# Performance work log

Hardware: AMD Instinct MI355X
Metric: run time of the kernel (lower is better)

Reference implementation:

```python
import jax, jax.numpy as jnp
import numpy as np

E, D, H, K = 8, 2048, 1024, 2  # num_experts, input_size, hidden_size, top_k
B, L = 2, 1024


def setup_inputs() -> dict:
    key = jax.random.key(0)
    k1, k2, k3, k4 = jax.random.split(key, 4)
    x = jax.random.normal(k1, (B, L, D), dtype=jnp.float32)
    w_gate = jax.random.normal(k2, (E, D), dtype=jnp.float32) * 0.02   # router Linear weight [E, D]
    w_in = jax.random.normal(k3, (E, 2 * H, D), dtype=jnp.float32) * 0.02  # ParallelExperts [E, out=2H, in=D]
    w_out = jax.random.normal(k4, (E, D, H), dtype=jnp.float32) * 0.02     # ParallelExperts [E, out=D, in=H]
    bias = jnp.zeros((D,), dtype=jnp.float32)
    return {"x": x, "w_gate": w_gate, "w_in": w_in, "w_out": w_out, "bias": bias}


def _moe_forward(x, w_gate, w_in, w_out, bias):
    bsz, length, d = x.shape
    xt = x.reshape(-1, d)  # [T, D]
    # top-k router: logits -> top-k -> softmax over selected logits
    logits = xt @ w_gate.T  # [T, E]
    topk_vals, topk_idx = jax.lax.top_k(logits, K)  # [T, K]
    topk_gates = jax.nn.softmax(topk_vals, axis=-1)  # [T, K]
    T = xt.shape[0]
    # dense [T, E] gate matrix; zero for non-selected experts, so the dense
    # per-expert compute below is mathematically identical to gathered dispatch
    gates = jnp.zeros((T, E), dtype=xt.dtype).at[jnp.arange(T)[:, None], topk_idx].add(topk_gates)
    # expert GLU FFN, vectorized over experts
    h = jnp.einsum('td,efd->tef', xt, w_in)  # [T, E, 2H]
    h1, h2 = jnp.split(h, 2, axis=-1)
    a = jax.nn.silu(h1) * h2                 # [T, E, H]
    eo = jnp.einsum('teh,edh->ted', a, w_out)  # [T, E, D]
    y = jnp.einsum('ted,te->td', eo, gates) + bias
    return y.reshape(bsz, length, d)


def reference(x, w_gate, w_in, w_out, bias):
    y = _moe_forward(x, w_gate, w_in, w_out, bias)
    loss = jnp.float32(0.0)  # router aux loss is 0 in eval mode (JetMoE top_k_gating)
    return (y, loss)
```

## Files before the change

kernel.cpp:

```cpp
#include <hip/hip_runtime.h>

#define E_    8
#define D_    2048
#define H_    1024
#define T_    2048
#define BK    64
#define NN    32

using u16   = unsigned short;
using s16x8 = __attribute__((ext_vector_type(8))) short;
using f32x4 = __attribute__((ext_vector_type(4))) float;

__device__ __forceinline__ u16 f2bf(float f) {
  union { float f; unsigned u; } v; v.f = f;
  unsigned r = v.u + 0x7fffu + ((v.u >> 16) & 1u);
  return (u16)(r >> 16);
}
__device__ __forceinline__ s16x8 cvt8(f32x4 a, f32x4 b) {
  s16x8 o;
  o[0]=(short)f2bf(a.x); o[1]=(short)f2bf(a.y); o[2]=(short)f2bf(a.z); o[3]=(short)f2bf(a.w);
  o[4]=(short)f2bf(b.x); o[5]=(short)f2bf(b.y); o[6]=(short)f2bf(b.z); o[7]=(short)f2bf(b.w);
  return o;
}
__device__ __forceinline__ int slot(int r, int c) { return r * 64 + ((c ^ (r & 7)) << 3); }

__device__ __forceinline__ void gload16(const void* g, void* l) {
  __builtin_amdgcn_global_load_lds((const __attribute__((address_space(1))) void*)g,
                                   (__attribute__((address_space(3))) void*)l, 16, 0, 0);
}

#define FIND_EXPERT(ml, cnt, e, mt, Ne)                        \
  { int b_ = 0;                                                \
    _Pragma("unroll")                                          \
    for (int i_ = 0; i_ < E_; ++i_) {                          \
      int ti_ = (cnt[i_] + 255) >> 8;                          \
      if ((ml) >= b_ && (ml) < b_ + ti_) {                     \
        e = i_; mt = (ml) - b_; Ne = cnt[i_]; }                \
      b_ += ti_; } }


__global__ __launch_bounds__(256) void init_kernel(
    const float* __restrict__ bias, float* __restrict__ out, int* __restrict__ counts)
{
  int idx = blockIdx.x * 256 + threadIdx.x;
  if (blockIdx.x == 0 && threadIdx.x < E_) counts[threadIdx.x] = 0;
  if (idx == 0) out[(size_t)T_ * D_] = 0.0f;
  int dq = idx & (D_ / 4 - 1);
  f32x4 b = *(const f32x4*)(bias + dq * 4);
  *(f32x4*)(out + (size_t)idx * 4) = b;
}

__global__ __launch_bounds__(256) void router_kernel(
    const float* __restrict__ x, const float* __restrict__ wg,
    u16* __restrict__ xb, int* __restrict__ lists, float* __restrict__ gates,
    int* __restrict__ counts)
{
  int t = blockIdx.x;
  int tid = threadIdx.x;
  const float* xr = x + (size_t)t * D_;
  float acc[E_];
#pragma unroll
  for (int e = 0; e < E_; ++e) acc[e] = 0.f;
#pragma unroll
  for (int i = 0; i < D_ / 256; ++i) {
    int d = tid + 256 * i;
    float xv = xr[d];
    xb[(size_t)t * D_ + d] = f2bf(xv);
#pragma unroll
    for (int e = 0; e < E_; ++e) acc[e] += xv * wg[e * D_ + d];
  }
#pragma unroll
  for (int off = 32; off >= 1; off >>= 1)
#pragma unroll
    for (int e = 0; e < E_; ++e) acc[e] += __shfl_down(acc[e], off);

  __shared__ float red[4][E_];
  int w = tid >> 6, lane = tid & 63;
  if (lane == 0)
#pragma unroll
    for (int e = 0; e < E_; ++e) red[w][e] = acc[e];
  __syncthreads();
  if (tid == 0) {
    float v0 = -1e30f, v1 = -1e30f; int e0 = 0, e1 = 0;
#pragma unroll
    for (int e = 0; e < E_; ++e) {
      float v = red[0][e] + red[1][e] + red[2][e] + red[3][e];
      if (v > v0)      { v1 = v0; e1 = e0; v0 = v; e0 = e; }
      else if (v > v1) { v1 = v;  e1 = e; }
    }
    float g1 = expf(v1 - v0);
    float inv = 1.f / (1.f + g1);
    float g0 = inv; g1 *= inv;
    int s0 = atomicAdd(&counts[e0], 1);
    lists[e0 * T_ + s0] = t * 2 + 0;
    gates[t * 2 + 0] = g0;
    int s1 = atomicAdd(&counts[e1], 1);
    lists[e1 * T_ + s1] = t * 2 + 1;
    gates[t * 2 + 1] = g1;
  }
}

__global__ __launch_bounds__(512, 4) void gemm1_kernel(
    const u16* __restrict__ xb, const float* __restrict__ w_in,
    const int* __restrict__ lists, const int* __restrict__ counts,
    u16* __restrict__ a_buf)
{
  __shared__ __align__(16) u16 As[2][256 * 64];
  __shared__ __align__(16) u16 Bs[2][64 * 64];

  int cnt[E_];
#pragma unroll
  for (int i = 0; i < E_; ++i) cnt[i] = counts[i];
  int mt_total = 0;
#pragma unroll
  for (int i = 0; i < E_; ++i) mt_total += (cnt[i] + 255) >> 8;
  int total = mt_total * NN;
  int chunk = (total + 7) >> 3;

  int tid = threadIdx.x, w = tid >> 6, lane = tid & 63;
  int swzc = ((lane & 7) ^ (lane >> 3)) * 8;
  int brow = tid >> 3, bch = tid & 7;
  int wr = (w >> 1) * 64, wcB = (w & 1) * 32, lrow = lane & 15, g = lane >> 4;
  int lcol = lane & 15, lr4 = (lane >> 4) * 4;

  int xcd = blockIdx.x & 7, bslot = blockIdx.x >> 3;

  for (int sl = bslot; sl < chunk; sl += 64) {
    int t = xcd * chunk + sl;
    if (t >= total) break;
    int ml = t >> 5, n = t & (NN - 1);
    int e = 0, mt = 0, Ne = 0;
    FIND_EXPERT(ml, cnt, e, mt, Ne);

    const u16* ap[4];
#pragma unroll
    for (int i = 0; i < 4; ++i) {
      int gr = mt * 256 + 32 * w + 8 * i + (lane >> 3);
      if (gr >= Ne) gr = Ne - 1;
      ap[i] = xb + (size_t)(lists[e * T_ + gr] >> 1) * D_ + swzc;
    }
    int o = n * 32 + ((brow >> 4) & 1) * H_ + (brow >> 5) * 16 + (brow & 15);
    const float* bp = w_in + (size_t)e * (2 * H_) * D_ + (size_t)o * D_ + bch * 8;

    f32x4 acc[4][2];
#pragma unroll
    for (int m = 0; m < 4; ++m) { acc[m][0] = (f32x4){0,0,0,0}; acc[m][1] = (f32x4){0,0,0,0}; }

    f32x4 bl0 = *(const f32x4*)(bp), bl1 = *(const f32x4*)(bp + 4);
#pragma unroll
    for (int i = 0; i < 4; ++i) gload16(ap[i], &As[0][(32 * w + 8 * i) * 64]);
    *(s16x8*)(&Bs[0][slot(brow, bch)]) = cvt8(bl0, bl1);
    __syncthreads();

    const int NT = D_ / BK;
    for (int kt = 0; kt < NT; ++kt) {
      int cur = kt & 1;
      if (kt + 1 < NT) {
        int k = (kt + 1) * BK;
        bl0 = *(const f32x4*)(bp + k); bl1 = *(const f32x4*)(bp + k + 4);
#pragma unroll
        for (int i = 0; i < 4; ++i) gload16(ap[i] + k, &As[cur ^ 1][(32 * w + 8 * i) * 64]);
      }
#pragma unroll
      for (int ks = 0; ks < 2; ++ks) {
        int ch = ks * 4 + g;
        s16x8 af[4], bf[2];
#pragma unroll
        for (int m = 0; m < 4; ++m) af[m] = *(const s16x8*)(&As[cur][slot(wr + m * 16 + lrow, ch)]);
#pragma unroll
        for (int nn = 0; nn < 2; ++nn) bf[nn] = *(const s16x8*)(&Bs[cur][slot(wcB + nn * 16 + lrow, ch)]);
#pragma unroll
        for (int m = 0; m < 4; ++m)
#pragma unroll
          for (int nn = 0; nn < 2; ++nn)
            acc[m][nn] = __builtin_amdgcn_mfma_f32_16x16x32_bf16(af[m], bf[nn], acc[m][nn], 0, 0, 0);
      }
      if (kt + 1 < NT)
        *(s16x8*)(&Bs[cur ^ 1][slot(brow, bch)]) = cvt8(bl0, bl1);
      __syncthreads();
    }
#pragma unroll
    for (int m = 0; m < 4; ++m)
#pragma unroll
      for (int q = 0; q < 4; ++q) {
        int row = mt * 256 + wr + m * 16 + lr4 + q;
        if (row < Ne) {
          float h1 = acc[m][0][q], h2 = acc[m][1][q];
          float a = (h1 / (1.f + __expf(-h1))) * h2;
          a_buf[((size_t)e * T_ + row) * H_ + n * 32 + (w & 1) * 16 + lcol] = f2bf(a);
        }
      }
  }
}

__global__ __launch_bounds__(512, 4) void gemm2_kernel(
    const u16* __restrict__ a_buf, const float* __restrict__ w_out,
    const int* __restrict__ lists, const int* __restrict__ counts,
    const float* __restrict__ gates, float* __restrict__ out)
{
  __shared__ __align__(16) u16 As[2][256 * 64];
  __shared__ __align__(16) u16 Bs[2][64 * 64];

  int cnt[E_];
#pragma unroll
  for (int i = 0; i < E_; ++i) cnt[i] = counts[i];
  int mt_total = 0;
#pragma unroll
  for (int i = 0; i < E_; ++i) mt_total += (cnt[i] + 255) >> 8;
  int total = mt_total * NN;
  int chunk = (total + 7) >> 3;

  int tid = threadIdx.x, w = tid >> 6, lane = tid & 63;
  int swzc = ((lane & 7) ^ (lane >> 3)) * 8;
  int brow = tid >> 3, bch = tid & 7;
  int wr = (w >> 1) * 64, wcB = (w & 1) * 32, lrow = lane & 15, g = lane >> 4;
  int lcol = lane & 15, lr4 = (lane >> 4) * 4;

  int xcd = blockIdx.x & 7, bslot = blockIdx.x >> 3;

  for (int sl = bslot; sl < chunk; sl += 64) {
    int t = xcd * chunk + sl;
    if (t >= total) break;
    int ml = t >> 5, n = t & (NN - 1);
    int e = 0, mt = 0, Ne = 0;
    FIND_EXPERT(ml, cnt, e, mt, Ne);

    const u16* ap[4];
#pragma unroll
    for (int i = 0; i < 4; ++i) {
      int gr = mt * 256 + 32 * w + 8 * i + (lane >> 3);
      if (gr >= Ne) gr = Ne - 1;
      ap[i] = a_buf + ((size_t)e * T_ + gr) * H_ + swzc;
    }
    const float* bp = w_out + (size_t)e * D_ * H_ + (size_t)(n * 64 + brow) * H_ + bch * 8;

    f32x4 acc[4][2];
#pragma unroll
    for (int m = 0; m < 4; ++m) { acc[m][0] = (f32x4){0,0,0,0}; acc[m][1] = (f32x4){0,0,0,0}; }

    f32x4 bl0 = *(const f32x4*)(bp), bl1 = *(const f32x4*)(bp + 4);
#pragma unroll
    for (int i = 0; i < 4; ++i) gload16(ap[i], &As[0][(32 * w + 8 * i) * 64]);
    *(s16x8*)(&Bs[0][slot(brow, bch)]) = cvt8(bl0, bl1);
    __syncthreads();

    const int NT = H_ / BK;
    for (int kt = 0; kt < NT; ++kt) {
      int cur = kt & 1;
      if (kt + 1 < NT) {
        int k = (kt + 1) * BK;
        bl0 = *(const f32x4*)(bp + k); bl1 = *(const f32x4*)(bp + k + 4);
#pragma unroll
        for (int i = 0; i < 4; ++i) gload16(ap[i] + k, &As[cur ^ 1][(32 * w + 8 * i) * 64]);
      }
#pragma unroll
      for (int ks = 0; ks < 2; ++ks) {
        int ch = ks * 4 + g;
        s16x8 af[4], bf[2];
#pragma unroll
        for (int m = 0; m < 4; ++m) af[m] = *(const s16x8*)(&As[cur][slot(wr + m * 16 + lrow, ch)]);
#pragma unroll
        for (int nn = 0; nn < 2; ++nn) bf[nn] = *(const s16x8*)(&Bs[cur][slot(wcB + nn * 16 + lrow, ch)]);
#pragma unroll
        for (int m = 0; m < 4; ++m)
#pragma unroll
          for (int nn = 0; nn < 2; ++nn)
            acc[m][nn] = __builtin_amdgcn_mfma_f32_16x16x32_bf16(af[m], bf[nn], acc[m][nn], 0, 0, 0);
      }
      if (kt + 1 < NT)
        *(s16x8*)(&Bs[cur ^ 1][slot(brow, bch)]) = cvt8(bl0, bl1);
      __syncthreads();
    }
#pragma unroll
    for (int m = 0; m < 4; ++m)
#pragma unroll
      for (int q = 0; q < 4; ++q) {
        int row = mt * 256 + wr + m * 16 + lr4 + q;
        if (row < Ne) {
          int p = lists[e * T_ + row];
          float gt = gates[p];
          int tok = p >> 1;
#pragma unroll
          for (int nn = 0; nn < 2; ++nn)
            atomicAdd(&out[(size_t)tok * D_ + n * 64 + wcB + nn * 16 + lcol], gt * acc[m][nn][q]);
        }
      }
  }
}

extern "C" void kernel_launch(void* const* d_in, const int* in_sizes, int n_in,
                              void* d_out, int out_size, void* d_ws, size_t ws_size,
                              hipStream_t stream)
{
  const float* x      = (const float*)d_in[0];
  const float* w_gate = (const float*)d_in[1];
  const float* w_in   = (const float*)d_in[2];
  const float* w_out  = (const float*)d_in[3];
  const float* bias   = (const float*)d_in[4];
  float* out = (float*)d_out;

  char* ws = (char*)d_ws;
  u16*   xb     = (u16*)(ws);
  u16*   a_buf  = (u16*)(ws + 8388608);
  int*   lists  = (int*)(ws + 41943040);
  float* gates  = (float*)(ws + 42008576);
  int*   counts = (int*)(ws + 42024960);

  init_kernel<<<T_ * D_ / 4 / 256, 256, 0, stream>>>(bias, out, counts);
  router_kernel<<<T_, 256, 0, stream>>>(x, w_gate, xb, lists, gates, counts);
  gemm1_kernel<<<512, 512, 0, stream>>>(xb, w_in, lists, counts, a_buf);
  gemm2_kernel<<<512, 512, 0, stream>>>(a_buf, w_out, lists, counts, gates, out);
}
```

Before: 231.2 us.

## Widen expert GEMM N-tile to 128 and halve grid size

Both expert GEMMs go from a 256x64 output tile to 256x128. Each warp now computes 4x4 MFMA accumulators, the B shared buffer doubles, and the grids and persistent stride drop from 512 to 256 blocks with launch bounds lowered to 2 blocks/SM. The aim is to halve how often each A tile (the gathered activations) is reloaded and to raise MFMA work per LDS read. The cost is more registers, more LDS, fewer resident waves, and coarser load balance across the reduced tile count. The bf16 conversion also switches to the HIP intrinsic __float2bfloat16.

```diff
diff --git a/kernel.cpp b/kernel.cpp
--- a/kernel.cpp
+++ b/kernel.cpp
@@ -1,25 +1,24 @@
 #include <hip/hip_runtime.h>
+#include <hip/hip_bf16.h>
 
 #define E_    8
 #define D_    2048
 #define H_    1024
 #define T_    2048
 #define BK    64
-#define NN    32
 
 using u16   = unsigned short;
 using s16x8 = __attribute__((ext_vector_type(8))) short;
 using f32x4 = __attribute__((ext_vector_type(4))) float;
 
-__device__ __forceinline__ u16 f2bf(float f) {
-  union { float f; unsigned u; } v; v.f = f;
-  unsigned r = v.u + 0x7fffu + ((v.u >> 16) & 1u);
-  return (u16)(r >> 16);
+__device__ __forceinline__ short f2bf(float f) {
+  __hip_bfloat16 h = __float2bfloat16(f);
+  return __builtin_bit_cast(short, h);
 }
 __device__ __forceinline__ s16x8 cvt8(f32x4 a, f32x4 b) {
   s16x8 o;
-  o[0]=(short)f2bf(a.x); o[1]=(short)f2bf(a.y); o[2]=(short)f2bf(a.z); o[3]=(short)f2bf(a.w);
-  o[4]=(short)f2bf(b.x); o[5]=(short)f2bf(b.y); o[6]=(short)f2bf(b.z); o[7]=(short)f2bf(b.w);
+  o[0]=f2bf(a.x); o[1]=f2bf(a.y); o[2]=f2bf(a.z); o[3]=f2bf(a.w);
+  o[4]=f2bf(b.x); o[5]=f2bf(b.y); o[6]=f2bf(b.z); o[7]=f2bf(b.w);
   return o;
 }
 __device__ __forceinline__ int slot(int r, int c) { return r * 64 + ((c ^ (r & 7)) << 3); }
@@ -65,7 +64,7 @@
   for (int i = 0; i < D_ / 256; ++i) {
     int d = tid + 256 * i;
     float xv = xr[d];
-    xb[(size_t)t * D_ + d] = f2bf(xv);
+    xb[(size_t)t * D_ + d] = (u16)f2bf(xv);
 #pragma unroll
     for (int e = 0; e < E_; ++e) acc[e] += xv * wg[e * D_ + d];
   }
@@ -100,13 +99,13 @@
   }
 }
 
-__global__ __launch_bounds__(512, 4) void gemm1_kernel(
+__global__ __launch_bounds__(512, 2) void gemm1_kernel(
     const u16* __restrict__ xb, const float* __restrict__ w_in,
     const int* __restrict__ lists, const int* __restrict__ counts,
     u16* __restrict__ a_buf)
 {
   __shared__ __align__(16) u16 As[2][256 * 64];
-  __shared__ __align__(16) u16 Bs[2][64 * 64];
+  __shared__ __align__(16) u16 Bs[2][128 * 64];
 
   int cnt[E_];
 #pragma unroll
@@ -114,21 +113,23 @@
   int mt_total = 0;
 #pragma unroll
   for (int i = 0; i < E_; ++i) mt_total += (cnt[i] + 255) >> 8;
-  int total = mt_total * NN;
+  const int NN1 = 2 * H_ / 128;
+  int total = mt_total * NN1;
   int chunk = (total + 7) >> 3;
 
   int tid = threadIdx.x, w = tid >> 6, lane = tid & 63;
   int swzc = ((lane & 7) ^ (lane >> 3)) * 8;
-  int brow = tid >> 3, bch = tid & 7;
-  int wr = (w >> 1) * 64, wcB = (w & 1) * 32, lrow = lane & 15, g = lane >> 4;
+  int sr = tid >> 3;
+  int brow = tid >> 2, bc = (tid & 3) * 2;
+  int wr = (w >> 1) * 64, wcB = (w & 1) * 64, lrow = lane & 15, g = lane >> 4;
   int lcol = lane & 15, lr4 = (lane >> 4) * 4;
 
   int xcd = blockIdx.x & 7, bslot = blockIdx.x >> 3;
 
-  for (int sl = bslot; sl < chunk; sl += 64) {
+  for (int sl = bslot; sl < chunk; sl += 32) {
     int t = xcd * chunk + sl;
     if (t >= total) break;
-    int ml = t >> 5, n = t & (NN - 1);
+    int ml = t / NN1, n = t % NN1;
     int e = 0, mt = 0, Ne = 0;
     FIND_EXPERT(ml, cnt, e, mt, Ne);
 
@@ -139,17 +140,24 @@
       if (gr >= Ne) gr = Ne - 1;
       ap[i] = xb + (size_t)(lists[e * T_ + gr] >> 1) * D_ + swzc;
     }
-    int o = n * 32 + ((brow >> 4) & 1) * H_ + (brow >> 5) * 16 + (brow & 15);
-    const float* bp = w_in + (size_t)e * (2 * H_) * D_ + (size_t)o * D_ + bch * 8;
-
-    f32x4 acc[4][2];
-#pragma unroll
-    for (int m = 0; m < 4; ++m) { acc[m][0] = (f32x4){0,0,0,0}; acc[m][1] = (f32x4){0,0,0,0}; }
-
-    f32x4 bl0 = *(const f32x4*)(bp), bl1 = *(const f32x4*)(bp + 4);
-#pragma unroll
-    for (int i = 0; i < 4; ++i) gload16(ap[i], &As[0][(32 * w + 8 * i) * 64]);
-    *(s16x8*)(&Bs[0][slot(brow, bch)]) = cvt8(bl0, bl1);
+    int o = n * 64 + ((brow >> 4) & 1) * H_ + (brow >> 5) * 16 + (brow & 15);
+    const float* bp = w_in + (size_t)e * (2 * H_) * D_ + (size_t)o * D_ + bc * 8;
+
+    f32x4 acc[4][4];
+#pragma unroll
+    for (int m = 0; m < 4; ++m)
+#pragma unroll
+      for (int nn = 0; nn < 4; ++nn) acc[m][nn] = (f32x4){0.f, 0.f, 0.f, 0.f};
+
+    f32x4 bl[4];
+#define LOADS1(K) { _Pragma("unroll") for (int j = 0; j < 4; ++j) \
+                      bl[j] = *(const f32x4*)(bp + (K) + j * 4); \
+                    _Pragma("unroll") for (int i = 0; i < 4; ++i) \
+                      gload16(ap[i] + (K), &As[(K) ? !((K/BK) & 1) : 0][(32 * w + 8 * i) * 64]); }
+    { _Pragma("unroll") for (int j = 0; j < 4; ++j) bl[j] = *(const f32x4*)(bp + j * 4);
+      _Pragma("unroll") for (int i = 0; i < 4; ++i) gload16(ap[i], &As[0][(32 * w + 8 * i) * 64]); }
+    *(s16x8*)(&Bs[0][slot(brow, bc)])     = cvt8(bl[0], bl[1]);
+    *(s16x8*)(&Bs[0][slot(brow, bc + 1)]) = cvt8(bl[2], bl[3]);
     __syncthreads();
 
     const int NT = D_ / BK;
@@ -157,26 +165,29 @@
       int cur = kt & 1;
       if (kt + 1 < NT) {
         int k = (kt + 1) * BK;
-        bl0 = *(const f32x4*)(bp + k); bl1 = *(const f32x4*)(bp + k + 4);
+#pragma unroll
+        for (int j = 0; j < 4; ++j) bl[j] = *(const f32x4*)(bp + k + j * 4);
 #pragma unroll
         for (int i = 0; i < 4; ++i) gload16(ap[i] + k, &As[cur ^ 1][(32 * w + 8 * i) * 64]);
       }
 #pragma unroll
       for (int ks = 0; ks < 2; ++ks) {
         int ch = ks * 4 + g;
-        s16x8 af[4], bf[2];
+        s16x8 af[4], bf[4];
 #pragma unroll
         for (int m = 0; m < 4; ++m) af[m] = *(const s16x8*)(&As[cur][slot(wr + m * 16 + lrow, ch)]);
 #pragma unroll
-        for (int nn = 0; nn < 2; ++nn) bf[nn] = *(const s16x8*)(&Bs[cur][slot(wcB + nn * 16 + lrow, ch)]);
+        for (int nn = 0; nn < 4; ++nn) bf[nn] = *(const s16x8*)(&Bs[cur][slot(wcB + nn * 16 + lrow, ch)]);
 #pragma unroll
         for (int m = 0; m < 4; ++m)
 #pragma unroll
-          for (int nn = 0; nn < 2; ++nn)
+          for (int nn = 0; nn < 4; ++nn)
             acc[m][nn] = __builtin_amdgcn_mfma_f32_16x16x32_bf16(af[m], bf[nn], acc[m][nn], 0, 0, 0);
       }
-      if (kt + 1 < NT)
-        *(s16x8*)(&Bs[cur ^ 1][slot(brow, bch)]) = cvt8(bl0, bl1);
+      if (kt + 1 < NT) {
+        *(s16x8*)(&Bs[cur ^ 1][slot(brow, bc)])     = cvt8(bl[0], bl[1]);
+        *(s16x8*)(&Bs[cur ^ 1][slot(brow, bc + 1)]) = cvt8(bl[2], bl[3]);
+      }
       __syncthreads();
     }
 #pragma unroll
@@ -185,21 +196,25 @@
       for (int q = 0; q < 4; ++q) {
         int row = mt * 256 + wr + m * 16 + lr4 + q;
         if (row < Ne) {
-          float h1 = acc[m][0][q], h2 = acc[m][1][q];
-          float a = (h1 / (1.f + __expf(-h1))) * h2;
-          a_buf[((size_t)e * T_ + row) * H_ + n * 32 + (w & 1) * 16 + lcol] = f2bf(a);
+#pragma unroll
+          for (int n2 = 0; n2 < 2; ++n2) {
+            float h1 = acc[m][n2 * 2][q], h2 = acc[m][n2 * 2 + 1][q];
+            float a = (h1 / (1.f + __expf(-h1))) * h2;
+            int col = n * 64 + ((w & 1) * 2 + n2) * 16 + lcol;
+            a_buf[((size_t)e * T_ + row) * H_ + col] = (u16)f2bf(a);
+          }
         }
       }
   }
 }
 
-__global__ __launch_bounds__(512, 4) void gemm2_kernel(
+__global__ __launch_bounds__(512, 2) void gemm2_kernel(
     const u16* __restrict__ a_buf, const float* __restrict__ w_out,
     const int* __restrict__ lists, const int* __restrict__ counts,
     const float* __restrict__ gates, float* __restrict__ out)
 {
   __shared__ __align__(16) u16 As[2][256 * 64];
-  __shared__ __align__(16) u16 Bs[2][64 * 64];
+  __shared__ __align__(16) u16 Bs[2][128 * 64];
 
   int cnt[E_];
 #pragma unroll
@@ -207,21 +222,22 @@
   int mt_total = 0;
 #pragma unroll
   for (int i = 0; i < E_; ++i) mt_total += (cnt[i] + 255) >> 8;
-  int total = mt_total * NN;
+  const int NN2 = D_ / 128;
+  int total = mt_total * NN2;
   int chunk = (total + 7) >> 3;
 
   int tid = threadIdx.x, w = tid >> 6, lane = tid & 63;
   int swzc = ((lane & 7) ^ (lane >> 3)) * 8;
-  int brow = tid >> 3, bch = tid & 7;
-  int wr = (w >> 1) * 64, wcB = (w & 1) * 32, lrow = lane & 15, g = lane >> 4;
+  int brow = tid >> 2, bc = (tid & 3) * 2;
+  int wr = (w >> 1) * 64, wcB = (w & 1) * 64, lrow = lane & 15, g = lane >> 4;
   int lcol = lane & 15, lr4 = (lane >> 4) * 4;
 
   int xcd = blockIdx.x & 7, bslot = blockIdx.x >> 3;
 
-  for (int sl = bslot; sl < chunk; sl += 64) {
+  for (int sl = bslot; sl < chunk; sl += 32) {
     int t = xcd * chunk + sl;
     if (t >= total) break;
-    int ml = t >> 5, n = t & (NN - 1);
+    int ml = t / NN2, n = t % NN2;
     int e = 0, mt = 0, Ne = 0;
     FIND_EXPERT(ml, cnt, e, mt, Ne);
 
@@ -232,16 +248,19 @@
       if (gr >= Ne) gr = Ne - 1;
       ap[i] = a_buf + ((size_t)e * T_ + gr) * H_ + swzc;
     }
-    const float* bp = w_out + (size_t)e * D_ * H_ + (size_t)(n * 64 + brow) * H_ + bch * 8;
-
-    f32x4 acc[4][2];
-#pragma unroll
-    for (int m = 0; m < 4; ++m) { acc[m][0] = (f32x4){0,0,0,0}; acc[m][1] = (f32x4){0,0,0,0}; }
-
-    f32x4 bl0 = *(const f32x4*)(bp), bl1 = *(const f32x4*)(bp + 4);
-#pragma unroll
-    for (int i = 0; i < 4; ++i) gload16(ap[i], &As[0][(32 * w + 8 * i) * 64]);
-    *(s16x8*)(&Bs[0][slot(brow, bch)]) = cvt8(bl0, bl1);
+    const float* bp = w_out + (size_t)e * D_ * H_ + (size_t)(n * 128 + brow) * H_ + bc * 8;
+
+    f32x4 acc[4][4];
+#pragma unroll
+    for (int m = 0; m < 4; ++m)
+#pragma unroll
+      for (int nn = 0; nn < 4; ++nn) acc[m][nn] = (f32x4){0.f, 0.f, 0.f, 0.f};
+
+    f32x4 bl[4];
+    { _Pragma("unroll") for (int j = 0; j < 4; ++j) bl[j] = *(const f32x4*)(bp + j * 4);
+      _Pragma("unroll") for (int i = 0; i < 4; ++i) gload16(ap[i], &As[0][(32 * w + 8 * i) * 64]); }
+    *(s16x8*)(&Bs[0][slot(brow, bc)])     = cvt8(bl[0], bl[1]);
+    *(s16x8*)(&Bs[0][slot(brow, bc + 1)]) = cvt8(bl[2], bl[3]);
     __syncthreads();
 
     const int NT = H_ / BK;
@@ -249,26 +268,29 @@
       int cur = kt & 1;
       if (kt + 1 < NT) {
         int k = (kt + 1) * BK;
-        bl0 = *(const f32x4*)(bp + k); bl1 = *(const f32x4*)(bp + k + 4);
+#pragma unroll
+        for (int j = 0; j < 4; ++j) bl[j] = *(const f32x4*)(bp + k + j * 4);
 #pragma unroll
         for (int i = 0; i < 4; ++i) gload16(ap[i] + k, &As[cur ^ 1][(32 * w + 8 * i) * 64]);
       }
 #pragma unroll
       for (int ks = 0; ks < 2; ++ks) {
         int ch = ks * 4 + g;
-        s16x8 af[4], bf[2];
+        s16x8 af[4], bf[4];
 #pragma unroll
         for (int m = 0; m < 4; ++m) af[m] = *(const s16x8*)(&As[cur][slot(wr + m * 16 + lrow, ch)]);
 #pragma unroll
-        for (int nn = 0; nn < 2; ++nn) bf[nn] = *(const s16x8*)(&Bs[cur][slot(wcB + nn * 16 + lrow, ch)]);
+        for (int nn = 0; nn < 4; ++nn) bf[nn] = *(const s16x8*)(&Bs[cur][slot(wcB + nn * 16 + lrow, ch)]);
 #pragma unroll
         for (int m = 0; m < 4; ++m)
 #pragma unroll
-          for (int nn = 0; nn < 2; ++nn)
+          for (int nn = 0; nn < 4; ++nn)
             acc[m][nn] = __builtin_amdgcn_mfma_f32_16x16x32_bf16(af[m], bf[nn], acc[m][nn], 0, 0, 0);
       }
-      if (kt + 1 < NT)
-        *(s16x8*)(&Bs[cur ^ 1][slot(brow, bch)]) = cvt8(bl0, bl1);
+      if (kt + 1 < NT) {
+        *(s16x8*)(&Bs[cur ^ 1][slot(brow, bc)])     = cvt8(bl[0], bl[1]);
+        *(s16x8*)(&Bs[cur ^ 1][slot(brow, bc + 1)]) = cvt8(bl[2], bl[3]);
+      }
       __syncthreads();
     }
 #pragma unroll
@@ -281,8 +303,8 @@
           float gt = gates[p];
           int tok = p >> 1;
 #pragma unroll
-          for (int nn = 0; nn < 2; ++nn)
-            atomicAdd(&out[(size_t)tok * D_ + n * 64 + wcB + nn * 16 + lcol], gt * acc[m][nn][q]);
+          for (int nn = 0; nn < 4; ++nn)
+            atomicAdd(&out[(size_t)tok * D_ + n * 128 + wcB + nn * 16 + lcol], gt * acc[m][nn][q]);
         }
       }
   }
@@ -308,6 +330,6 @@
 
   init_kernel<<<T_ * D_ / 4 / 256, 256, 0, stream>>>(bias, out, counts);
   router_kernel<<<T_, 256, 0, stream>>>(x, w_gate, xb, lists, gates, counts);
-  gemm1_kernel<<<512, 512, 0, stream>>>(xb, w_in, lists, counts, a_buf);
-  gemm2_kernel<<<512, 512, 0, stream>>>(a_buf, w_out, lists, counts, gates, out);
-}
+  gemm1_kernel<<<256, 512, 0, stream>>>(xb, w_in, lists, counts, a_buf);
+  gemm2_kernel<<<256, 512, 0, stream>>>(a_buf, w_out, lists, counts, gates, out);
+}
```

Measured after the change: 265.8 us. +15.0%, slower.

## Pre-convert expert weights to bf16 and load both GEMM operands via direct LDS DMA

Applied to the files above, without the earlier changes.

A fused prep kernel now converts w_in and w_out to bf16 in workspace, writes the bias into the output and runs the router, replacing the separate init kernel (counts are zeroed with a memset). Both GEMMs then stream A and B tiles straight into LDS with global_load_lds using a square 128x128 tile, instead of loading fp32 weights into registers and converting them every k-step. This removes the per-tile conversion and register staging, and the output tile becomes more square for better reuse. The cost is an extra full-weight read and bf16 write on every call, a larger workspace, and explicit vmcnt waits before each barrier.

```diff
diff --git a/kernel.cpp b/kernel.cpp
--- a/kernel.cpp
+++ b/kernel.cpp
@@ -1,26 +1,21 @@
 #include <hip/hip_runtime.h>
+#include <hip/hip_bf16.h>
 
 #define E_    8
 #define D_    2048
 #define H_    1024
 #define T_    2048
 #define BK    64
-#define NN    32
 
 using u16   = unsigned short;
 using s16x8 = __attribute__((ext_vector_type(8))) short;
 using f32x4 = __attribute__((ext_vector_type(4))) float;
 
-__device__ __forceinline__ u16 f2bf(float f) {
-  union { float f; unsigned u; } v; v.f = f;
-  unsigned r = v.u + 0x7fffu + ((v.u >> 16) & 1u);
-  return (u16)(r >> 16);
-}
-__device__ __forceinline__ s16x8 cvt8(f32x4 a, f32x4 b) {
-  s16x8 o;
-  o[0]=(short)f2bf(a.x); o[1]=(short)f2bf(a.y); o[2]=(short)f2bf(a.z); o[3]=(short)f2bf(a.w);
-  o[4]=(short)f2bf(b.x); o[5]=(short)f2bf(b.y); o[6]=(short)f2bf(b.z); o[7]=(short)f2bf(b.w);
-  return o;
+#define WAITVM0 asm volatile("s_waitcnt vmcnt(0)" ::: "memory")
+
+__device__ __forceinline__ short f2bf(float f) {
+  __hip_bfloat16 h = __float2bfloat16(f);
+  return __builtin_bit_cast(short, h);
 }
 __device__ __forceinline__ int slot(int r, int c) { return r * 64 + ((c ^ (r & 7)) << 3); }
 
@@ -33,30 +28,48 @@
   { int b_ = 0;                                                \
     _Pragma("unroll")                                          \
     for (int i_ = 0; i_ < E_; ++i_) {                          \
-      int ti_ = (cnt[i_] + 255) >> 8;                          \
+      int ti_ = (cnt[i_] + 127) >> 7;                          \
       if ((ml) >= b_ && (ml) < b_ + ti_) {                     \
         e = i_; mt = (ml) - b_; Ne = cnt[i_]; }                \
       b_ += ti_; } }
 
 
-__global__ __launch_bounds__(256) void init_kernel(
-    const float* __restrict__ bias, float* __restrict__ out, int* __restrict__ counts)
-{
-  int idx = blockIdx.x * 256 + threadIdx.x;
-  if (blockIdx.x == 0 && threadIdx.x < E_) counts[threadIdx.x] = 0;
-  if (idx == 0) out[(size_t)T_ * D_] = 0.0f;
-  int dq = idx & (D_ / 4 - 1);
-  f32x4 b = *(const f32x4*)(bias + dq * 4);
-  *(f32x4*)(out + (size_t)idx * 4) = b;
-}
-
-__global__ __launch_bounds__(256) void router_kernel(
+#define WIN_ELEMS  33554432
+#define WTOT_ELEMS 50331648
+
+__global__ __launch_bounds__(256) void prep_kernel(
     const float* __restrict__ x, const float* __restrict__ wg,
-    u16* __restrict__ xb, int* __restrict__ lists, float* __restrict__ gates,
-    int* __restrict__ counts)
+    const float* __restrict__ w_in, const float* __restrict__ w_out,
+    const float* __restrict__ bias,
+    u16* __restrict__ xb, u16* __restrict__ wb_in, u16* __restrict__ wb_out,
+    int* __restrict__ lists, float* __restrict__ gates, int* __restrict__ counts,
+    float* __restrict__ out)
 {
   int t = blockIdx.x;
   int tid = threadIdx.x;
+
+#pragma unroll
+  for (int j = 0; j < 12; ++j) {
+    int idx = t * 24576 + j * 2048 + tid * 8;
+    const float* src; u16* dst;
+    if (idx < WIN_ELEMS) { src = w_in + idx;  dst = wb_in + idx; }
+    else                 { src = w_out + (idx - WIN_ELEMS); dst = wb_out + (idx - WIN_ELEMS); }
+    f32x4 a = *(const f32x4*)(src);
+    f32x4 b = *(const f32x4*)(src + 4);
+    s16x8 o;
+    o[0]=f2bf(a.x); o[1]=f2bf(a.y); o[2]=f2bf(a.z); o[3]=f2bf(a.w);
+    o[4]=f2bf(b.x); o[5]=f2bf(b.y); o[6]=f2bf(b.z); o[7]=f2bf(b.w);
+    *(s16x8*)dst = o;
+  }
+
+  {
+    const float* bp = bias + tid * 8;
+    f32x4 b0 = *(const f32x4*)(bp), b1 = *(const f32x4*)(bp + 4);
+    *(f32x4*)(out + (size_t)t * D_ + tid * 8)     = b0;
+    *(f32x4*)(out + (size_t)t * D_ + tid * 8 + 4) = b1;
+    if (t == 0 && tid == 0) out[(size_t)T_ * D_] = 0.0f;
+  }
+
   const float* xr = x + (size_t)t * D_;
   float acc[E_];
 #pragma unroll
@@ -65,7 +78,7 @@
   for (int i = 0; i < D_ / 256; ++i) {
     int d = tid + 256 * i;
     float xv = xr[d];
-    xb[(size_t)t * D_ + d] = f2bf(xv);
+    xb[(size_t)t * D_ + d] = (u16)f2bf(xv);
 #pragma unroll
     for (int e = 0; e < E_; ++e) acc[e] += xv * wg[e * D_ + d];
   }
@@ -100,56 +113,61 @@
   }
 }
 
-__global__ __launch_bounds__(512, 4) void gemm1_kernel(
-    const u16* __restrict__ xb, const float* __restrict__ w_in,
+__global__ __launch_bounds__(512, 2) void gemm1_kernel(
+    const u16* __restrict__ xb, const u16* __restrict__ wb_in,
     const int* __restrict__ lists, const int* __restrict__ counts,
     u16* __restrict__ a_buf)
 {
-  __shared__ __align__(16) u16 As[2][256 * 64];
-  __shared__ __align__(16) u16 Bs[2][64 * 64];
+  __shared__ __align__(16) u16 As[2][128 * 64];
+  __shared__ __align__(16) u16 Bs[2][128 * 64];
 
   int cnt[E_];
 #pragma unroll
   for (int i = 0; i < E_; ++i) cnt[i] = counts[i];
   int mt_total = 0;
 #pragma unroll
-  for (int i = 0; i < E_; ++i) mt_total += (cnt[i] + 255) >> 8;
-  int total = mt_total * NN;
+  for (int i = 0; i < E_; ++i) mt_total += (cnt[i] + 127) >> 7;
+  int total = mt_total * 16;
   int chunk = (total + 7) >> 3;
 
   int tid = threadIdx.x, w = tid >> 6, lane = tid & 63;
   int swzc = ((lane & 7) ^ (lane >> 3)) * 8;
-  int brow = tid >> 3, bch = tid & 7;
-  int wr = (w >> 1) * 64, wcB = (w & 1) * 32, lrow = lane & 15, g = lane >> 4;
+  int wr = (w >> 2) * 64, wc = (w & 3) * 32, lrow = lane & 15, g = lane >> 4;
   int lcol = lane & 15, lr4 = (lane >> 4) * 4;
-
   int xcd = blockIdx.x & 7, bslot = blockIdx.x >> 3;
 
   for (int sl = bslot; sl < chunk; sl += 64) {
     int t = xcd * chunk + sl;
     if (t >= total) break;
-    int ml = t >> 5, n = t & (NN - 1);
+    int ml = t >> 4, n = t & 15;
     int e = 0, mt = 0, Ne = 0;
     FIND_EXPERT(ml, cnt, e, mt, Ne);
 
-    const u16* ap[4];
-#pragma unroll
-    for (int i = 0; i < 4; ++i) {
-      int gr = mt * 256 + 32 * w + 8 * i + (lane >> 3);
+    const u16* ap[2];
+#pragma unroll
+    for (int i = 0; i < 2; ++i) {
+      int gr = mt * 128 + w * 8 + i * 64 + (lane >> 3);
       if (gr >= Ne) gr = Ne - 1;
       ap[i] = xb + (size_t)(lists[e * T_ + gr] >> 1) * D_ + swzc;
     }
-    int o = n * 32 + ((brow >> 4) & 1) * H_ + (brow >> 5) * 16 + (brow & 15);
-    const float* bp = w_in + (size_t)e * (2 * H_) * D_ + (size_t)o * D_ + bch * 8;
+    const u16* bp[2];
+#pragma unroll
+    for (int i = 0; i < 2; ++i) {
+      int br = w * 8 + i * 64 + (lane >> 3);
+      int o = n * 64 + ((br >> 4) & 1) * H_ + (br >> 5) * 16 + (br & 15);
+      bp[i] = wb_in + (size_t)e * (2 * H_) * D_ + (size_t)o * D_ + swzc;
+    }
 
     f32x4 acc[4][2];
 #pragma unroll
     for (int m = 0; m < 4; ++m) { acc[m][0] = (f32x4){0,0,0,0}; acc[m][1] = (f32x4){0,0,0,0}; }
 
-    f32x4 bl0 = *(const f32x4*)(bp), bl1 = *(const f32x4*)(bp + 4);
-#pragma unroll
-    for (int i = 0; i < 4; ++i) gload16(ap[i], &As[0][(32 * w + 8 * i) * 64]);
-    *(s16x8*)(&Bs[0][slot(brow, bch)]) = cvt8(bl0, bl1);
+#pragma unroll
+    for (int i = 0; i < 2; ++i) {
+      gload16(ap[i], &As[0][(w * 8 + i * 64) * 64]);
+      gload16(bp[i], &Bs[0][(w * 8 + i * 64) * 64]);
+    }
+    WAITVM0;
     __syncthreads();
 
     const int NT = D_ / BK;
@@ -157,9 +175,11 @@
       int cur = kt & 1;
       if (kt + 1 < NT) {
         int k = (kt + 1) * BK;
-        bl0 = *(const f32x4*)(bp + k); bl1 = *(const f32x4*)(bp + k + 4);
-#pragma unroll
-        for (int i = 0; i < 4; ++i) gload16(ap[i] + k, &As[cur ^ 1][(32 * w + 8 * i) * 64]);
+#pragma unroll
+        for (int i = 0; i < 2; ++i) {
+          gload16(ap[i] + k, &As[cur ^ 1][(w * 8 + i * 64) * 64]);
+          gload16(bp[i] + k, &Bs[cur ^ 1][(w * 8 + i * 64) * 64]);
+        }
       }
 #pragma unroll
       for (int ks = 0; ks < 2; ++ks) {
@@ -168,80 +188,84 @@
 #pragma unroll
         for (int m = 0; m < 4; ++m) af[m] = *(const s16x8*)(&As[cur][slot(wr + m * 16 + lrow, ch)]);
 #pragma unroll
-        for (int nn = 0; nn < 2; ++nn) bf[nn] = *(const s16x8*)(&Bs[cur][slot(wcB + nn * 16 + lrow, ch)]);
+        for (int s = 0; s < 2; ++s)  bf[s] = *(const s16x8*)(&Bs[cur][slot(wc + s * 16 + lrow, ch)]);
 #pragma unroll
         for (int m = 0; m < 4; ++m)
 #pragma unroll
-          for (int nn = 0; nn < 2; ++nn)
-            acc[m][nn] = __builtin_amdgcn_mfma_f32_16x16x32_bf16(af[m], bf[nn], acc[m][nn], 0, 0, 0);
-      }
-      if (kt + 1 < NT)
-        *(s16x8*)(&Bs[cur ^ 1][slot(brow, bch)]) = cvt8(bl0, bl1);
+          for (int s = 0; s < 2; ++s)
+            acc[m][s] = __builtin_amdgcn_mfma_f32_16x16x32_bf16(af[m], bf[s], acc[m][s], 0, 0, 0);
+      }
+      WAITVM0;
       __syncthreads();
     }
 #pragma unroll
     for (int m = 0; m < 4; ++m)
 #pragma unroll
       for (int q = 0; q < 4; ++q) {
-        int row = mt * 256 + wr + m * 16 + lr4 + q;
+        int row = mt * 128 + wr + m * 16 + lr4 + q;
         if (row < Ne) {
           float h1 = acc[m][0][q], h2 = acc[m][1][q];
           float a = (h1 / (1.f + __expf(-h1))) * h2;
-          a_buf[((size_t)e * T_ + row) * H_ + n * 32 + (w & 1) * 16 + lcol] = f2bf(a);
+          a_buf[((size_t)e * T_ + row) * H_ + n * 64 + (w & 3) * 16 + lcol] = (u16)f2bf(a);
         }
       }
   }
 }
 
-__global__ __launch_bounds__(512, 4) void gemm2_kernel(
-    const u16* __restrict__ a_buf, const float* __restrict__ w_out,
+__global__ __launch_bounds__(512, 2) void gemm2_kernel(
+    const u16* __restrict__ a_buf, const u16* __restrict__ wb_out,
     const int* __restrict__ lists, const int* __restrict__ counts,
     const float* __restrict__ gates, float* __restrict__ out)
 {
-  __shared__ __align__(16) u16 As[2][256 * 64];
-  __shared__ __align__(16) u16 Bs[2][64 * 64];
+  __shared__ __align__(16) u16 As[2][128 * 64];
+  __shared__ __align__(16) u16 Bs[2][128 * 64];
 
   int cnt[E_];
 #pragma unroll
   for (int i = 0; i < E_; ++i) cnt[i] = counts[i];
   int mt_total = 0;
 #pragma unroll
-  for (int i = 0; i < E_; ++i) mt_total += (cnt[i] + 255) >> 8;
-  int total = mt_total * NN;
+  for (int i = 0; i < E_; ++i) mt_total += (cnt[i] + 127) >> 7;
+  int total = mt_total * 16;
   int chunk = (total + 7) >> 3;
 
   int tid = threadIdx.x, w = tid >> 6, lane = tid & 63;
   int swzc = ((lane & 7) ^ (lane >> 3)) * 8;
-  int brow = tid >> 3, bch = tid & 7;
-  int wr = (w >> 1) * 64, wcB = (w & 1) * 32, lrow = lane & 15, g = lane >> 4;
+  int wr = (w >> 2) * 64, wc = (w & 3) * 32, lrow = lane & 15, g = lane >> 4;
   int lcol = lane & 15, lr4 = (lane >> 4) * 4;
-
   int xcd = blockIdx.x & 7, bslot = blockIdx.x >> 3;
 
   for (int sl = bslot; sl < chunk; sl += 64) {
     int t = xcd * chunk + sl;
     if (t >= total) break;
-    int ml = t >> 5, n = t & (NN - 1);
+    int ml = t >> 4, n = t & 15;
     int e = 0, mt = 0, Ne = 0;
     FIND_EXPERT(ml, cnt, e, mt, Ne);
 
-    const u16* ap[4];
-#pragma unroll
-    for (int i = 0; i < 4; ++i) {
-      int gr = mt * 256 + 32 * w + 8 * i + (lane >> 3);
+    const u16* ap[2];
+#pragma unroll
+    for (int i = 0; i < 2; ++i) {
+      int gr = mt * 128 + w * 8 + i * 64 + (lane >> 3);
       if (gr >= Ne) gr = Ne - 1;
       ap[i] = a_buf + ((size_t)e * T_ + gr) * H_ + swzc;
     }
-    const float* bp = w_out + (size_t)e * D_ * H_ + (size_t)(n * 64 + brow) * H_ + bch * 8;
+    const u16* bp[2];
+#pragma unroll
+    for (int i = 0; i < 2; ++i) {
+      int br = w * 8 + i * 64 + (lane >> 3);
+      bp[i] = wb_out + (size_t)e * D_ * H_ + (size_t)(n * 128 + br) * H_ + swzc;
+    }
 
     f32x4 acc[4][2];
 #pragma unroll
     for (int m = 0; m < 4; ++m) { acc[m][0] = (f32x4){0,0,0,0}; acc[m][1] = (f32x4){0,0,0,0}; }
 
-    f32x4 bl0 = *(const f32x4*)(bp), bl1 = *(const f32x4*)(bp + 4);
-#pragma unroll
-    for (int i = 0; i < 4; ++i) gload16(ap[i], &As[0][(32 * w + 8 * i) * 64]);
-    *(s16x8*)(&Bs[0][slot(brow, bch)]) = cvt8(bl0, bl1);
+#pragma unroll
+    for (int i = 0; i < 2; ++i) {
+      gload16(ap[i], &As[0][(w * 8 + i * 64) * 64]);
+      gload16(bp[i], &Bs[0][(w * 8 + i * 64) * 64]);
+    }
+    WAITVM0;
     __syncthreads();
 
     const int NT = H_ / BK;
@@ -249,9 +273,11 @@
       int cur = kt & 1;
       if (kt + 1 < NT) {
         int k = (kt + 1) * BK;
-        bl0 = *(const f32x4*)(bp + k); bl1 = *(const f32x4*)(bp + k + 4);
-#pragma unroll
-        for (int i = 0; i < 4; ++i) gload16(ap[i] + k, &As[cur ^ 1][(32 * w + 8 * i) * 64]);
+#pragma unroll
+        for (int i = 0; i < 2; ++i) {
+          gload16(ap[i] + k, &As[cur ^ 1][(w * 8 + i * 64) * 64]);
+          gload16(bp[i] + k, &Bs[cur ^ 1][(w * 8 + i * 64) * 64]);
+        }
       }
 #pragma unroll
       for (int ks = 0; ks < 2; ++ks) {
@@ -260,29 +286,28 @@
 #pragma unroll
         for (int m = 0; m < 4; ++m) af[m] = *(const s16x8*)(&As[cur][slot(wr + m * 16 + lrow, ch)]);
 #pragma unroll
-        for (int nn = 0; nn < 2; ++nn) bf[nn] = *(const s16x8*)(&Bs[cur][slot(wcB + nn * 16 + lrow, ch)]);
+        for (int s = 0; s < 2; ++s)  bf[s] = *(const s16x8*)(&Bs[cur][slot(wc + s * 16 + lrow, ch)]);
 #pragma unroll
         for (int m = 0; m < 4; ++m)
 #pragma unroll
-          for (int nn = 0; nn < 2; ++nn)
-            acc[m][nn] = __builtin_amdgcn_mfma_f32_16x16x32_bf16(af[m], bf[nn], acc[m][nn], 0, 0, 0);
-      }
-      if (kt + 1 < NT)
-        *(s16x8*)(&Bs[cur ^ 1][slot(brow, bch)]) = cvt8(bl0, bl1);
+          for (int s = 0; s < 2; ++s)
+            acc[m][s] = __builtin_amdgcn_mfma_f32_16x16x32_bf16(af[m], bf[s], acc[m][s], 0, 0, 0);
+      }
+      WAITVM0;
       __syncthreads();
     }
 #pragma unroll
     for (int m = 0; m < 4; ++m)
 #pragma unroll
       for (int q = 0; q < 4; ++q) {
-        int row = mt * 256 + wr + m * 16 + lr4 + q;
+        int row = mt * 128 + wr + m * 16 + lr4 + q;
         if (row < Ne) {
           int p = lists[e * T_ + row];
           float gt = gates[p];
           int tok = p >> 1;
 #pragma unroll
-          for (int nn = 0; nn < 2; ++nn)
-            atomicAdd(&out[(size_t)tok * D_ + n * 64 + wcB + nn * 16 + lcol], gt * acc[m][nn][q]);
+          for (int s = 0; s < 2; ++s)
+            atomicAdd(&out[(size_t)tok * D_ + n * 128 + wc + s * 16 + lcol], gt * acc[m][s][q]);
         }
       }
   }
@@ -302,12 +327,15 @@
   char* ws = (char*)d_ws;
   u16*   xb     = (u16*)(ws);
   u16*   a_buf  = (u16*)(ws + 8388608);
-  int*   lists  = (int*)(ws + 41943040);
-  float* gates  = (float*)(ws + 42008576);
-  int*   counts = (int*)(ws + 42024960);
-
-  init_kernel<<<T_ * D_ / 4 / 256, 256, 0, stream>>>(bias, out, counts);
-  router_kernel<<<T_, 256, 0, stream>>>(x, w_gate, xb, lists, gates, counts);
-  gemm1_kernel<<<512, 512, 0, stream>>>(xb, w_in, lists, counts, a_buf);
-  gemm2_kernel<<<512, 512, 0, stream>>>(a_buf, w_out, lists, counts, gates, out);
-}
+  u16*   wb_in  = (u16*)(ws + 41943040);
+  u16*   wb_out = (u16*)(ws + 109051904);
+  int*   lists  = (int*)(ws + 142606336);
+  float* gates  = (float*)(ws + 142671872);
+  int*   counts = (int*)(ws + 142688256);
+
+  hipMemsetAsync(counts, 0, E_ * sizeof(int), stream);
+  prep_kernel<<<T_, 256, 0, stream>>>(x, w_gate, w_in, w_out, bias,
+                                      xb, wb_in, wb_out, lists, gates, counts, out);
+  gemm1_kernel<<<512, 512, 0, stream>>>(xb, wb_in, lists, counts, a_buf);
+  gemm2_kernel<<<512, 512, 0, stream>>>(a_buf, wb_out, lists, counts, gates, out);
+}
```

New measurement: 226.8 us. No clear change (-1.9%).
